# Kernel optimization log

Hardware: AMD Instinct MI355X
Metric: run time of the kernel (lower is better)

Reference implementation:

```python
import jax, jax.numpy as jnp
import numpy as np

N_EMBD = 384
BLOCK_SIZE = 256

def setup_inputs() -> dict:
    key = jax.random.key(0)
    k1, k2 = jax.random.split(key)
    B, T = 512, 256
    x = jax.random.normal(k1, (B, T, N_EMBD), dtype=jnp.float32)
    # nn.Linear(384, 192, bias=False): store as [in, out] so projection is x @ w
    w_qkv = jax.random.normal(k2, (N_EMBD, 3 * 64), dtype=jnp.float32) * (1.0 / np.sqrt(N_EMBD))
    return {"x": x, "w_qkv": w_qkv}

def reference(x, w_qkv):
    B, T, C = x.shape  # C == n_embd == 384
    qkv = jnp.einsum('btc,cd->btd', x, w_qkv)       # [B,T,3*hs]
    q, k, v = jnp.split(qkv, 3, axis=-1)            # each [B,T,hs]
    scale = 1.0 / jnp.sqrt(jnp.float32(C))          # NOTE: scales by full embed dim C, per source
    wei = jnp.einsum('btd,bsd->bts', q, k) * scale  # [B,T,T]
    causal = jnp.tril(jnp.ones((T, T), dtype=bool))
    wei = jnp.where(causal, wei, -jnp.inf)
    wei = jax.nn.softmax(wei, axis=-1)
    # dropout is identity in eval mode
    return jnp.einsum('bts,bsd->btd', wei, v)       # [B,T,hs]
```

## Files before the change

### kernel.cpp

```cpp
#include <hip/hip_runtime.h>


constexpr int B  = 512;
constexpr int T  = 256;
constexpr int C  = 384;
constexpr int HS = 64;
constexpr int NT = 192;
constexpr int BK = 64;
constexpr int NKC = C / BK;
constexpr int ROWP = 72;
constexpr int VP   = 264;
constexpr float SCALE = 0.05103103630798288f;
constexpr float QSC   = SCALE * 1.4426950408889634f;

typedef _Float16 f16x8 __attribute__((ext_vector_type(8)));
typedef _Float16 f16x4 __attribute__((ext_vector_type(4)));
typedef __fp16   fp16x2_raw __attribute__((ext_vector_type(2)));
typedef float    f32x4 __attribute__((ext_vector_type(4)));

__global__ __launch_bounds__(256)
void wt_kernel(const float* __restrict__ w, _Float16* __restrict__ wt) {
    const int idx = blockIdx.x * 256 + threadIdx.x;
    if (idx < NT * C) {
        const int n = idx / C, k = idx % C;
        wt[idx] = (_Float16)w[k * NT + n];
    }
}

__global__ __launch_bounds__(512)
void fused_kernel(const float* __restrict__ x, const _Float16* __restrict__ wt,
                  float* __restrict__ out) {
    __shared__ __align__(16) _Float16 XL[T * ROWP];
    __shared__ __align__(16) _Float16 WL[NT * BK];
    __shared__ __align__(16) _Float16 QL[T * HS];
    __shared__ __align__(16) _Float16 KL[T * HS];
    __shared__ __align__(16) _Float16 VTL[HS * VP];

    const int tid  = threadIdx.x;
    const int lane = tid & 63, wv = tid >> 6;
    const int l15  = lane & 15, quad = lane >> 4;
    const int wm   = wv >> 1, wn = wv & 1;
    const float* xb = x + (long)blockIdx.x * T * C;

    f32x4 acc[4][6];
#pragma unroll
    for (int mi = 0; mi < 4; ++mi)
#pragma unroll
        for (int ni = 0; ni < 6; ++ni) acc[mi][ni] = (f32x4)0.f;

    float4 xv[8];
    uint4  wvr[3];
#pragma unroll
    for (int i = 0; i < 8; ++i) {
        const int flat = tid + 512 * i, r = flat >> 4, seg = flat & 15;
        xv[i] = *(const float4*)(xb + r * C + seg * 4);
    }
#pragma unroll
    for (int i = 0; i < 3; ++i) {
        const int u = tid + 512 * i, n = u >> 3, sl = u & 7;
        wvr[i] = *(const uint4*)(wt + n * C + sl * 8);
    }

    for (int kc = 0; kc < NKC; ++kc) {
        __syncthreads();
#pragma unroll
        for (int i = 0; i < 8; ++i) {
            const int flat = tid + 512 * i, r = flat >> 4, seg = flat & 15;
            union { fp16x2_raw h[2]; uint2 u; } cv;
            cv.h[0] = __builtin_amdgcn_cvt_pkrtz(xv[i].x, xv[i].y);
            cv.h[1] = __builtin_amdgcn_cvt_pkrtz(xv[i].z, xv[i].w);
            *(uint2*)&XL[r * ROWP + seg * 4] = cv.u;
        }
#pragma unroll
        for (int i = 0; i < 3; ++i) {
            const int u = tid + 512 * i, n = u >> 3, sl = u & 7;
            *(uint4*)&WL[n * BK + ((sl ^ (n & 7)) << 3)] = wvr[i];
        }
        __syncthreads();
        if (kc + 1 < NKC) {
            const int k0 = (kc + 1) * BK;
#pragma unroll
            for (int i = 0; i < 8; ++i) {
                const int flat = tid + 512 * i, r = flat >> 4, seg = flat & 15;
                xv[i] = *(const float4*)(xb + r * C + k0 + seg * 4);
            }
#pragma unroll
            for (int i = 0; i < 3; ++i) {
                const int u = tid + 512 * i, n = u >> 3, sl = u & 7;
                wvr[i] = *(const uint4*)(wt + n * C + k0 + sl * 8);
            }
        }
#pragma unroll
        for (int s = 0; s < 2; ++s) {
            const int kk = s * 32 + quad * 8;
            const int slot = kk >> 3;
            f16x8 a[4], bf[6];
#pragma unroll
            for (int mi = 0; mi < 4; ++mi)
                a[mi] = *(const f16x8*)&XL[(wm * 64 + mi * 16 + l15) * ROWP + kk];
#pragma unroll
            for (int ni = 0; ni < 6; ++ni) {
                const int row = wn * 96 + ni * 16 + l15;
                bf[ni] = *(const f16x8*)&WL[row * BK + ((slot ^ (row & 7)) << 3)];
            }
#pragma unroll
            for (int mi = 0; mi < 4; ++mi)
#pragma unroll
                for (int ni = 0; ni < 6; ++ni)
                    acc[mi][ni] = __builtin_amdgcn_mfma_f32_16x16x32_f16(
                        a[mi], bf[ni], acc[mi][ni], 0, 0, 0);
        }
    }

#pragma unroll
    for (int mi = 0; mi < 4; ++mi) {
        const int t0 = wm * 64 + mi * 16 + quad * 4;
#pragma unroll
        for (int ni = 0; ni < 6; ++ni) {
            const int colbase = wn * 96 + ni * 16;
            const int col = colbase + l15;
            if (colbase < 64) {
#pragma unroll
                for (int r = 0; r < 4; ++r) {
                    const int t = t0 + r;
                    QL[(t * HS + col) ^ ((t & 7) << 3)] =
                        (_Float16)(acc[mi][ni][r] * QSC);
                }
            } else if (colbase < 128) {
#pragma unroll
                for (int r = 0; r < 4; ++r) {
                    const int t = t0 + r;
                    KL[(t * HS + (col - 64)) ^ ((t & 7) << 3)] =
                        (_Float16)acc[mi][ni][r];
                }
            } else {
                f16x4 pv;
#pragma unroll
                for (int r = 0; r < 4; ++r) pv[r] = (_Float16)acc[mi][ni][r];
                *(f16x4*)&VTL[(col - 128) * VP + t0] = pv;
            }
        }
    }
    __syncthreads();

    float* ob = out + (long)blockIdx.x * T * HS;
#pragma unroll
    for (int pass = 0; pass < 2; ++pass) {
        const int ch = pass ? (15 - wv) : wv;
        const int q0 = ch * 16;
        const int qrow = q0 + l15;
        const f16x8 qf0 = *(const f16x8*)&QL[(qrow * HS + quad * 8) ^ ((qrow & 7) << 3)];
        const f16x8 qf1 = *(const f16x8*)&QL[(qrow * HS + 32 + quad * 8) ^ ((qrow & 7) << 3)];
        f32x4 o[4];
#pragma unroll
        for (int di = 0; di < 4; ++di) o[di] = (f32x4)0.f;
        float lp = 0.f;

        for (int kt = 0; kt <= ch; ++kt) {
            const int k0 = kt * 16;
            const int krow = k0 + l15;
            const f16x8 ka0 = *(const f16x8*)&KL[(krow * HS + quad * 8) ^ ((krow & 7) << 3)];
            const f16x8 ka1 = *(const f16x8*)&KL[(krow * HS + 32 + quad * 8) ^ ((krow & 7) << 3)];
            f16x4 va[4];
#pragma unroll
            for (int di = 0; di < 4; ++di)
                va[di] = *(const f16x4*)&VTL[(di * 16 + l15) * VP + k0 + quad * 4];

            f32x4 s = {0.f, 0.f, 0.f, 0.f};
            s = __builtin_amdgcn_mfma_f32_16x16x32_f16(ka0, qf0, s, 0, 0, 0);
            s = __builtin_amdgcn_mfma_f32_16x16x32_f16(ka1, qf1, s, 0, 0, 0);

            const bool dmask = (kt == ch);
            f16x4 pb; float psum = 0.f;
#pragma unroll
            for (int r = 0; r < 4; ++r) {
                float pr = exp2f(s[r]);
                pr = (dmask && (quad * 4 + r > l15)) ? 0.f : pr;
                psum += pr;
                pb[r] = (_Float16)pr;
            }
            lp += psum;
#pragma unroll
            for (int di = 0; di < 4; ++di)
                o[di] = __builtin_amdgcn_mfma_f32_16x16x16f16(va[di], pb, o[di], 0, 0, 0);
        }

        float v = lp;
        v += __shfl_xor(v, 16, 64);
        v += __shfl_xor(v, 32, 64);
        const float inv = 1.0f / v;
#pragma unroll
        for (int di = 0; di < 4; ++di) {
            float4 val;
            val.x = o[di][0] * inv; val.y = o[di][1] * inv;
            val.z = o[di][2] * inv; val.w = o[di][3] * inv;
            *(float4*)&ob[qrow * HS + di * 16 + quad * 4] = val;
        }
    }
}

extern "C" void kernel_launch(void* const* d_in, const int* in_sizes, int n_in,
                              void* d_out, int out_size, void* d_ws, size_t ws_size,
                              hipStream_t stream) {
    const float* x = (const float*)d_in[0];
    const float* w = (const float*)d_in[1];
    float* out = (float*)d_out;

    _Float16* wt = (_Float16*)d_ws;

    wt_kernel<<<dim3((NT * C + 255) / 256), dim3(256), 0, stream>>>(w, wt);
    fused_kernel<<<dim3(B), dim3(512), 0, stream>>>(x, wt, out);
}
```

Measured before the change: 311.7 us.

## Process two batches per block with cross-batch prefetch and raw exp2

```diff
diff --git a/kernel.cpp b/kernel.cpp
--- a/kernel.cpp
+++ b/kernel.cpp
@@ -18,6 +18,15 @@
 typedef __fp16   fp16x2_raw __attribute__((ext_vector_type(2)));
 typedef float    f32x4 __attribute__((ext_vector_type(4)));
 
+#if defined(__has_builtin)
+#if __has_builtin(__builtin_amdgcn_exp2f)
+#define EXP2F(v) __builtin_amdgcn_exp2f(v)
+#endif
+#endif
+#ifndef EXP2F
+#define EXP2F(v) exp2f(v)
+#endif
+
 __global__ __launch_bounds__(256)
 void wt_kernel(const float* __restrict__ w, _Float16* __restrict__ wt) {
     const int idx = blockIdx.x * 256 + threadIdx.x;
@@ -40,161 +49,173 @@
     const int lane = tid & 63, wv = tid >> 6;
     const int l15  = lane & 15, quad = lane >> 4;
     const int wm   = wv >> 1, wn = wv & 1;
-    const float* xb = x + (long)blockIdx.x * T * C;
-
-    f32x4 acc[4][6];
-#pragma unroll
-    for (int mi = 0; mi < 4; ++mi)
-#pragma unroll
-        for (int ni = 0; ni < 6; ++ni) acc[mi][ni] = (f32x4)0.f;
+    const long b0  = (long)blockIdx.x * 2;
 
     float4 xv[8];
     uint4  wvr[3];
-#pragma unroll
-    for (int i = 0; i < 8; ++i) {
-        const int flat = tid + 512 * i, r = flat >> 4, seg = flat & 15;
-        xv[i] = *(const float4*)(xb + r * C + seg * 4);
-    }
-#pragma unroll
-    for (int i = 0; i < 3; ++i) {
-        const int u = tid + 512 * i, n = u >> 3, sl = u & 7;
-        wvr[i] = *(const uint4*)(wt + n * C + sl * 8);
-    }
-
-    for (int kc = 0; kc < NKC; ++kc) {
-        __syncthreads();
+    {
+        const float* xs = x + b0 * T * C;
 #pragma unroll
         for (int i = 0; i < 8; ++i) {
             const int flat = tid + 512 * i, r = flat >> 4, seg = flat & 15;
-            union { fp16x2_raw h[2]; uint2 u; } cv;
-            cv.h[0] = __builtin_amdgcn_cvt_pkrtz(xv[i].x, xv[i].y);
-            cv.h[1] = __builtin_amdgcn_cvt_pkrtz(xv[i].z, xv[i].w);
-            *(uint2*)&XL[r * ROWP + seg * 4] = cv.u;
+            xv[i] = *(const float4*)(xs + r * C + seg * 4);
         }
 #pragma unroll
         for (int i = 0; i < 3; ++i) {
             const int u = tid + 512 * i, n = u >> 3, sl = u & 7;
-            *(uint4*)&WL[n * BK + ((sl ^ (n & 7)) << 3)] = wvr[i];
-        }
-        __syncthreads();
-        if (kc + 1 < NKC) {
-            const int k0 = (kc + 1) * BK;
+            wvr[i] = *(const uint4*)(wt + n * C + sl * 8);
+        }
+    }
+
+#pragma unroll
+    for (int bi = 0; bi < 2; ++bi) {
+        const float* xbb = x + (b0 + bi) * T * C;
+
+        f32x4 acc[4][6];
+#pragma unroll
+        for (int mi = 0; mi < 4; ++mi)
+#pragma unroll
+            for (int ni = 0; ni < 6; ++ni) acc[mi][ni] = (f32x4)0.f;
+
+        for (int kc = 0; kc < NKC; ++kc) {
+            __syncthreads();
 #pragma unroll
             for (int i = 0; i < 8; ++i) {
                 const int flat = tid + 512 * i, r = flat >> 4, seg = flat & 15;
-                xv[i] = *(const float4*)(xb + r * C + k0 + seg * 4);
+                union { fp16x2_raw h[2]; uint2 u; } cv;
+                cv.h[0] = __builtin_amdgcn_cvt_pkrtz(xv[i].x, xv[i].y);
+                cv.h[1] = __builtin_amdgcn_cvt_pkrtz(xv[i].z, xv[i].w);
+                *(uint2*)&XL[r * ROWP + seg * 4] = cv.u;
             }
 #pragma unroll
             for (int i = 0; i < 3; ++i) {
                 const int u = tid + 512 * i, n = u >> 3, sl = u & 7;
-                wvr[i] = *(const uint4*)(wt + n * C + k0 + sl * 8);
-            }
-        }
-#pragma unroll
-        for (int s = 0; s < 2; ++s) {
-            const int kk = s * 32 + quad * 8;
-            const int slot = kk >> 3;
-            f16x8 a[4], bf[6];
-#pragma unroll
-            for (int mi = 0; mi < 4; ++mi)
-                a[mi] = *(const f16x8*)&XL[(wm * 64 + mi * 16 + l15) * ROWP + kk];
+                *(uint4*)&WL[n * BK + ((sl ^ (n & 7)) << 3)] = wvr[i];
+            }
+            __syncthreads();
+
+            const bool last = (kc == NKC - 1);
+            if (!last || bi == 0) {
+                const float*    px = last ? xbb + (long)T * C : xbb + (kc + 1) * BK;
+                const _Float16* pw = wt + (last ? 0 : (kc + 1) * BK);
+#pragma unroll
+                for (int i = 0; i < 8; ++i) {
+                    const int flat = tid + 512 * i, r = flat >> 4, seg = flat & 15;
+                    xv[i] = *(const float4*)(px + r * C + seg * 4);
+                }
+#pragma unroll
+                for (int i = 0; i < 3; ++i) {
+                    const int u = tid + 512 * i, n = u >> 3, sl = u & 7;
+                    wvr[i] = *(const uint4*)(pw + n * C + sl * 8);
+                }
+            }
+
+#pragma unroll
+            for (int s = 0; s < 2; ++s) {
+                const int kk = s * 32 + quad * 8;
+                const int slot = kk >> 3;
+                f16x8 a[4], bf[6];
+#pragma unroll
+                for (int mi = 0; mi < 4; ++mi)
+                    a[mi] = *(const f16x8*)&XL[(wm * 64 + mi * 16 + l15) * ROWP + kk];
+#pragma unroll
+                for (int ni = 0; ni < 6; ++ni) {
+                    const int row = wn * 96 + ni * 16 + l15;
+                    bf[ni] = *(const f16x8*)&WL[row * BK + ((slot ^ (row & 7)) << 3)];
+                }
+#pragma unroll
+                for (int mi = 0; mi < 4; ++mi)
+#pragma unroll
+                    for (int ni = 0; ni < 6; ++ni)
+                        acc[mi][ni] = __builtin_amdgcn_mfma_f32_16x16x32_f16(
+                            a[mi], bf[ni], acc[mi][ni], 0, 0, 0);
+            }
+        }
+
+#pragma unroll
+        for (int mi = 0; mi < 4; ++mi) {
+            const int t0 = wm * 64 + mi * 16 + quad * 4;
 #pragma unroll
             for (int ni = 0; ni < 6; ++ni) {
-                const int row = wn * 96 + ni * 16 + l15;
-                bf[ni] = *(const f16x8*)&WL[row * BK + ((slot ^ (row & 7)) << 3)];
-            }
-#pragma unroll
-            for (int mi = 0; mi < 4; ++mi)
-#pragma unroll
-                for (int ni = 0; ni < 6; ++ni)
-                    acc[mi][ni] = __builtin_amdgcn_mfma_f32_16x16x32_f16(
-                        a[mi], bf[ni], acc[mi][ni], 0, 0, 0);
-        }
-    }
-
-#pragma unroll
-    for (int mi = 0; mi < 4; ++mi) {
-        const int t0 = wm * 64 + mi * 16 + quad * 4;
-#pragma unroll
-        for (int ni = 0; ni < 6; ++ni) {
-            const int colbase = wn * 96 + ni * 16;
-            const int col = colbase + l15;
-            if (colbase < 64) {
+                const int colbase = wn * 96 + ni * 16;
+                const int col = colbase + l15;
+                if (colbase < 64) {
+#pragma unroll
+                    for (int r = 0; r < 4; ++r) {
+                        const int t = t0 + r;
+                        QL[(t * HS + col) ^ ((t & 7) << 3)] =
+                            (_Float16)(acc[mi][ni][r] * QSC);
+                    }
+                } else if (colbase < 128) {
+#pragma unroll
+                    for (int r = 0; r < 4; ++r) {
+                        const int t = t0 + r;
+                        KL[(t * HS + (col - 64)) ^ ((t & 7) << 3)] =
+                            (_Float16)acc[mi][ni][r];
+                    }
+                } else {
+                    f16x4 pv;
+#pragma unroll
+                    for (int r = 0; r < 4; ++r) pv[r] = (_Float16)acc[mi][ni][r];
+                    *(f16x4*)&VTL[(col - 128) * VP + t0] = pv;
+                }
+            }
+        }
+        __syncthreads();
+
+        float* ob = out + (b0 + bi) * T * HS;
+#pragma unroll
+        for (int pass = 0; pass < 2; ++pass) {
+            const int ch = pass ? (15 - wv) : wv;
+            const int q0 = ch * 16;
+            const int qrow = q0 + l15;
+            const f16x8 qf0 = *(const f16x8*)&QL[(qrow * HS + quad * 8) ^ ((qrow & 7) << 3)];
+            const f16x8 qf1 = *(const f16x8*)&QL[(qrow * HS + 32 + quad * 8) ^ ((qrow & 7) << 3)];
+            f32x4 o[4];
+#pragma unroll
+            for (int di = 0; di < 4; ++di) o[di] = (f32x4)0.f;
+            float lp = 0.f;
+
+            for (int kt = 0; kt <= ch; ++kt) {
+                const int k0 = kt * 16;
+                const int krow = k0 + l15;
+                const f16x8 ka0 = *(const f16x8*)&KL[(krow * HS + quad * 8) ^ ((krow & 7) << 3)];
+                const f16x8 ka1 = *(const f16x8*)&KL[(krow * HS + 32 + quad * 8) ^ ((krow & 7) << 3)];
+                f16x4 va[4];
+#pragma unroll
+                for (int di = 0; di < 4; ++di)
+                    va[di] = *(const f16x4*)&VTL[(di * 16 + l15) * VP + k0 + quad * 4];
+
+                f32x4 s = {0.f, 0.f, 0.f, 0.f};
+                s = __builtin_amdgcn_mfma_f32_16x16x32_f16(ka0, qf0, s, 0, 0, 0);
+                s = __builtin_amdgcn_mfma_f32_16x16x32_f16(ka1, qf1, s, 0, 0, 0);
+
+                const bool dmask = (kt == ch);
+                f16x4 pb; float psum = 0.f;
 #pragma unroll
                 for (int r = 0; r < 4; ++r) {
-                    const int t = t0 + r;
-                    QL[(t * HS + col) ^ ((t & 7) << 3)] =
-                        (_Float16)(acc[mi][ni][r] * QSC);
-                }
-            } else if (colbase < 128) {
-#pragma unroll
-                for (int r = 0; r < 4; ++r) {
-                    const int t = t0 + r;
-                    KL[(t * HS + (col - 64)) ^ ((t & 7) << 3)] =
-                        (_Float16)acc[mi][ni][r];
-                }
-            } else {
-                f16x4 pv;
-#pragma unroll
-                for (int r = 0; r < 4; ++r) pv[r] = (_Float16)acc[mi][ni][r];
-                *(f16x4*)&VTL[(col - 128) * VP + t0] = pv;
-            }
-        }
-    }
-    __syncthreads();
-
-    float* ob = out + (long)blockIdx.x * T * HS;
-#pragma unroll
-    for (int pass = 0; pass < 2; ++pass) {
-        const int ch = pass ? (15 - wv) : wv;
-        const int q0 = ch * 16;
-        const int qrow = q0 + l15;
-        const f16x8 qf0 = *(const f16x8*)&QL[(qrow * HS + quad * 8) ^ ((qrow & 7) << 3)];
-        const f16x8 qf1 = *(const f16x8*)&QL[(qrow * HS + 32 + quad * 8) ^ ((qrow & 7) << 3)];
-        f32x4 o[4];
-#pragma unroll
-        for (int di = 0; di < 4; ++di) o[di] = (f32x4)0.f;
-        float lp = 0.f;
-
-        for (int kt = 0; kt <= ch; ++kt) {
-            const int k0 = kt * 16;
-            const int krow = k0 + l15;
-            const f16x8 ka0 = *(const f16x8*)&KL[(krow * HS + quad * 8) ^ ((krow & 7) << 3)];
-            const f16x8 ka1 = *(const f16x8*)&KL[(krow * HS + 32 + quad * 8) ^ ((krow & 7) << 3)];
-            f16x4 va[4];
-#pragma unroll
-            for (int di = 0; di < 4; ++di)
-                va[di] = *(const f16x4*)&VTL[(di * 16 + l15) * VP + k0 + quad * 4];
-
-            f32x4 s = {0.f, 0.f, 0.f, 0.f};
-            s = __builtin_amdgcn_mfma_f32_16x16x32_f16(ka0, qf0, s, 0, 0, 0);
-            s = __builtin_amdgcn_mfma_f32_16x16x32_f16(ka1, qf1, s, 0, 0, 0);
-
-            const bool dmask = (kt == ch);
-            f16x4 pb; float psum = 0.f;
-#pragma unroll
-            for (int r = 0; r < 4; ++r) {
-                float pr = exp2f(s[r]);
-                pr = (dmask && (quad * 4 + r > l15)) ? 0.f : pr;
-                psum += pr;
-                pb[r] = (_Float16)pr;
-            }
-            lp += psum;
-#pragma unroll
-            for (int di = 0; di < 4; ++di)
-                o[di] = __builtin_amdgcn_mfma_f32_16x16x16f16(va[di], pb, o[di], 0, 0, 0);
-        }
-
-        float v = lp;
-        v += __shfl_xor(v, 16, 64);
-        v += __shfl_xor(v, 32, 64);
-        const float inv = 1.0f / v;
-#pragma unroll
-        for (int di = 0; di < 4; ++di) {
-            float4 val;
-            val.x = o[di][0] * inv; val.y = o[di][1] * inv;
-            val.z = o[di][2] * inv; val.w = o[di][3] * inv;
-            *(float4*)&ob[qrow * HS + di * 16 + quad * 4] = val;
+                    float pr = EXP2F(s[r]);
+                    pr = (dmask && (quad * 4 + r > l15)) ? 0.f : pr;
+                    psum += pr;
+                    pb[r] = (_Float16)pr;
+                }
+                lp += psum;
+#pragma unroll
+                for (int di = 0; di < 4; ++di)
+                    o[di] = __builtin_amdgcn_mfma_f32_16x16x16f16(va[di], pb, o[di], 0, 0, 0);
+            }
+
+            float v = lp;
+            v += __shfl_xor(v, 16, 64);
+            v += __shfl_xor(v, 32, 64);
+            const float inv = 1.0f / v;
+#pragma unroll
+            for (int di = 0; di < 4; ++di) {
+                float4 val;
+                val.x = o[di][0] * inv; val.y = o[di][1] * inv;
+                val.z = o[di][2] * inv; val.w = o[di][3] * inv;
+                *(float4*)&ob[qrow * HS + di * 16 + quad * 4] = val;
+            }
         }
     }
 }
@@ -209,5 +230,5 @@
     _Float16* wt = (_Float16*)d_ws;
 
     wt_kernel<<<dim3((NT * C + 255) / 256), dim3(256), 0, stream>>>(w, wt);
-    fused_kernel<<<dim3(B), dim3(512), 0, stream>>>(x, wt, out);
+    fused_kernel<<<dim3(B / 2), dim3(512), 0, stream>>>(x, wt, out);
 }
```

New measurement: 314.8 us. No clear change (+1.0%).

## Keep full weight matrix in LDS and stream x directly into MFMA registers

Applied to the files above, without the earlier changes.

```diff
diff --git a/kernel.cpp b/kernel.cpp
--- a/kernel.cpp
+++ b/kernel.cpp
@@ -6,10 +6,7 @@
 constexpr int C  = 384;
 constexpr int HS = 64;
 constexpr int NT = 192;
-constexpr int BK = 64;
-constexpr int NKC = C / BK;
-constexpr int ROWP = 72;
-constexpr int VP   = 264;
+constexpr int VP = 264;
 constexpr float SCALE = 0.05103103630798288f;
 constexpr float QSC   = SCALE * 1.4426950408889634f;
 
@@ -17,6 +14,15 @@
 typedef _Float16 f16x4 __attribute__((ext_vector_type(4)));
 typedef __fp16   fp16x2_raw __attribute__((ext_vector_type(2)));
 typedef float    f32x4 __attribute__((ext_vector_type(4)));
+
+#if defined(__has_builtin)
+#if __has_builtin(__builtin_amdgcn_exp2f)
+#define EXP2F(v) __builtin_amdgcn_exp2f(v)
+#endif
+#endif
+#ifndef EXP2F
+#define EXP2F(v) exp2f(v)
+#endif
 
 __global__ __launch_bounds__(256)
 void wt_kernel(const float* __restrict__ w, _Float16* __restrict__ wt) {
@@ -30,107 +36,96 @@
 __global__ __launch_bounds__(512)
 void fused_kernel(const float* __restrict__ x, const _Float16* __restrict__ wt,
                   float* __restrict__ out) {
-    __shared__ __align__(16) _Float16 XL[T * ROWP];
-    __shared__ __align__(16) _Float16 WL[NT * BK];
-    __shared__ __align__(16) _Float16 QL[T * HS];
-    __shared__ __align__(16) _Float16 KL[T * HS];
-    __shared__ __align__(16) _Float16 VTL[HS * VP];
+    __shared__ __align__(16) char arena[NT * C * 2];
+    _Float16* const QL  = (_Float16*)arena;
+    _Float16* const KL  = (_Float16*)(arena + 32768);
+    _Float16* const VTL = (_Float16*)(arena + 65536);
 
     const int tid  = threadIdx.x;
     const int lane = tid & 63, wv = tid >> 6;
     const int l15  = lane & 15, quad = lane >> 4;
-    const int wm   = wv >> 1, wn = wv & 1;
+    const int swz  = (l15 & 7) << 4;
+    const int q16  = quad << 4;
     const float* xb = x + (long)blockIdx.x * T * C;
 
-    f32x4 acc[4][6];
-#pragma unroll
-    for (int mi = 0; mi < 4; ++mi)
-#pragma unroll
-        for (int ni = 0; ni < 6; ++ni) acc[mi][ni] = (f32x4)0.f;
-
-    float4 xv[8];
-    uint4  wvr[3];
-#pragma unroll
-    for (int i = 0; i < 8; ++i) {
-        const int flat = tid + 512 * i, r = flat >> 4, seg = flat & 15;
-        xv[i] = *(const float4*)(xb + r * C + seg * 4);
-    }
-#pragma unroll
-    for (int i = 0; i < 3; ++i) {
-        const int u = tid + 512 * i, n = u >> 3, sl = u & 7;
-        wvr[i] = *(const uint4*)(wt + n * C + sl * 8);
-    }
-
-    for (int kc = 0; kc < NKC; ++kc) {
-        __syncthreads();
-#pragma unroll
-        for (int i = 0; i < 8; ++i) {
-            const int flat = tid + 512 * i, r = flat >> 4, seg = flat & 15;
-            union { fp16x2_raw h[2]; uint2 u; } cv;
-            cv.h[0] = __builtin_amdgcn_cvt_pkrtz(xv[i].x, xv[i].y);
-            cv.h[1] = __builtin_amdgcn_cvt_pkrtz(xv[i].z, xv[i].w);
-            *(uint2*)&XL[r * ROWP + seg * 4] = cv.u;
-        }
-#pragma unroll
-        for (int i = 0; i < 3; ++i) {
-            const int u = tid + 512 * i, n = u >> 3, sl = u & 7;
-            *(uint4*)&WL[n * BK + ((sl ^ (n & 7)) << 3)] = wvr[i];
-        }
-        __syncthreads();
-        if (kc + 1 < NKC) {
-            const int k0 = (kc + 1) * BK;
-#pragma unroll
-            for (int i = 0; i < 8; ++i) {
-                const int flat = tid + 512 * i, r = flat >> 4, seg = flat & 15;
-                xv[i] = *(const float4*)(xb + r * C + k0 + seg * 4);
-            }
-#pragma unroll
-            for (int i = 0; i < 3; ++i) {
-                const int u = tid + 512 * i, n = u >> 3, sl = u & 7;
-                wvr[i] = *(const uint4*)(wt + n * C + k0 + sl * 8);
-            }
-        }
-#pragma unroll
-        for (int s = 0; s < 2; ++s) {
-            const int kk = s * 32 + quad * 8;
-            const int slot = kk >> 3;
-            f16x8 a[4], bf[6];
-#pragma unroll
-            for (int mi = 0; mi < 4; ++mi)
-                a[mi] = *(const f16x8*)&XL[(wm * 64 + mi * 16 + l15) * ROWP + kk];
-#pragma unroll
-            for (int ni = 0; ni < 6; ++ni) {
-                const int row = wn * 96 + ni * 16 + l15;
-                bf[ni] = *(const f16x8*)&WL[row * BK + ((slot ^ (row & 7)) << 3)];
-            }
-#pragma unroll
-            for (int mi = 0; mi < 4; ++mi)
-#pragma unroll
-                for (int ni = 0; ni < 6; ++ni)
-                    acc[mi][ni] = __builtin_amdgcn_mfma_f32_16x16x32_f16(
-                        a[mi], bf[ni], acc[mi][ni], 0, 0, 0);
-        }
-    }
-
-#pragma unroll
-    for (int mi = 0; mi < 4; ++mi) {
-        const int t0 = wm * 64 + mi * 16 + quad * 4;
-#pragma unroll
-        for (int ni = 0; ni < 6; ++ni) {
-            const int colbase = wn * 96 + ni * 16;
+#pragma unroll
+    for (int i = 0; i < 18; ++i) {
+        const int u = tid + 512 * i;
+        const int n = u / 48, sl = u - n * 48;
+        const uint4 wv4 = *(const uint4*)((const char*)wt + (long)u * 16);
+        *(uint4*)(arena + n * 768 + ((sl * 16) ^ ((n & 7) << 4))) = wv4;
+    }
+
+    const float* pA0 = xb + (wv * 32 + l15) * C + quad * 8;
+    const float* pA1 = xb + (wv * 32 + 16 + l15) * C + quad * 8;
+
+    f32x4 ax[2][2][2];
+    ax[0][0][0] = *(const f32x4*)(pA0 + 0);
+    ax[0][0][1] = *(const f32x4*)(pA0 + 4);
+    ax[0][1][0] = *(const f32x4*)(pA1 + 0);
+    ax[0][1][1] = *(const f32x4*)(pA1 + 4);
+
+    f32x4 acc[2][12];
+#pragma unroll
+    for (int mi = 0; mi < 2; ++mi)
+#pragma unroll
+        for (int ni = 0; ni < 12; ++ni) acc[mi][ni] = (f32x4)0.f;
+
+    int rowb[12];
+#pragma unroll
+    for (int ni = 0; ni < 12; ++ni) rowb[ni] = (ni * 16 + l15) * 768;
+
+    __syncthreads();
+
+#pragma unroll
+    for (int t = 0; t < 12; ++t) {
+        const int cur = t & 1, nxt = cur ^ 1;
+        if (t < 11) {
+            ax[nxt][0][0] = *(const f32x4*)(pA0 + (t + 1) * 32);
+            ax[nxt][0][1] = *(const f32x4*)(pA0 + (t + 1) * 32 + 4);
+            ax[nxt][1][0] = *(const f32x4*)(pA1 + (t + 1) * 32);
+            ax[nxt][1][1] = *(const f32x4*)(pA1 + (t + 1) * 32 + 4);
+        }
+        f16x8 af[2];
+#pragma unroll
+        for (int mi = 0; mi < 2; ++mi) {
+            union { fp16x2_raw h[4]; f16x8 v; } cu;
+            cu.h[0] = __builtin_amdgcn_cvt_pkrtz(ax[cur][mi][0][0], ax[cur][mi][0][1]);
+            cu.h[1] = __builtin_amdgcn_cvt_pkrtz(ax[cur][mi][0][2], ax[cur][mi][0][3]);
+            cu.h[2] = __builtin_amdgcn_cvt_pkrtz(ax[cur][mi][1][0], ax[cur][mi][1][1]);
+            cu.h[3] = __builtin_amdgcn_cvt_pkrtz(ax[cur][mi][1][2], ax[cur][mi][1][3]);
+            af[mi] = cu.v;
+        }
+        const int col = ((t * 64) + q16) ^ swz;
+#pragma unroll
+        for (int ni = 0; ni < 12; ++ni) {
+            const f16x8 bf = *(const f16x8*)(arena + rowb[ni] + col);
+            acc[0][ni] = __builtin_amdgcn_mfma_f32_16x16x32_f16(af[0], bf, acc[0][ni], 0, 0, 0);
+            acc[1][ni] = __builtin_amdgcn_mfma_f32_16x16x32_f16(af[1], bf, acc[1][ni], 0, 0, 0);
+        }
+    }
+
+    __syncthreads();
+
+#pragma unroll
+    for (int mi = 0; mi < 2; ++mi) {
+        const int t0 = wv * 32 + mi * 16 + quad * 4;
+#pragma unroll
+        for (int ni = 0; ni < 12; ++ni) {
+            const int colbase = ni * 16;
             const int col = colbase + l15;
             if (colbase < 64) {
 #pragma unroll
                 for (int r = 0; r < 4; ++r) {
-                    const int t = t0 + r;
-                    QL[(t * HS + col) ^ ((t & 7) << 3)] =
+                    const int tq = t0 + r;
+                    QL[(tq * HS + col) ^ ((tq & 7) << 3)] =
                         (_Float16)(acc[mi][ni][r] * QSC);
                 }
             } else if (colbase < 128) {
 #pragma unroll
                 for (int r = 0; r < 4; ++r) {
-                    const int t = t0 + r;
-                    KL[(t * HS + (col - 64)) ^ ((t & 7) << 3)] =
+                    const int tq = t0 + r;
+                    KL[(tq * HS + (col - 64)) ^ ((tq & 7) << 3)] =
                         (_Float16)acc[mi][ni][r];
                 }
             } else {
@@ -174,7 +169,7 @@
             f16x4 pb; float psum = 0.f;
 #pragma unroll
             for (int r = 0; r < 4; ++r) {
-                float pr = exp2f(s[r]);
+                float pr = EXP2F(s[r]);
                 pr = (dmask && (quad * 4 + r > l15)) ? 0.f : pr;
                 psum += pr;
                 pb[r] = (_Float16)pr;
```

Measured after the change: 299.6 us. -3.9%, faster.
